# Performance work log

Hardware: AMD Instinct MI355X
Metric: run time of the kernel (lower is better)

## Reference

```python
import jax, jax.numpy as jnp
import numpy as np

C = 1024
H = 16
EPS = 1e-5

def layernorm(x, g, b):
    mu = jnp.mean(x, axis=-1, keepdims=True)
    var = jnp.var(x, axis=-1, keepdims=True)
    return (x - mu) * jax.lax.rsqrt(var + EPS) * g + b

def setup_inputs() -> dict:
    key = jax.random.key(0)
    ks = jax.random.split(key, 12)
    s = lambda fan: 1.0 / np.sqrt(fan)
    return {
        "x": jax.random.normal(ks[0], (2, 2048, C), jnp.float32),
        "W_qkv": jax.random.uniform(ks[1], (C, 3 * C), jnp.float32, -s(C), s(C)),
        "W_o": jax.random.uniform(ks[2], (C, C), jnp.float32, -s(C), s(C)),
        "b_o": jnp.zeros((C,), jnp.float32),
        "g1": jnp.ones((C,), jnp.float32),
        "beta1": jnp.zeros((C,), jnp.float32),
        "g2": jnp.ones((C,), jnp.float32),
        "beta2": jnp.zeros((C,), jnp.float32),
        "W_ff1": jax.random.uniform(ks[3], (C, 4 * C), jnp.float32, -s(C), s(C)),
        "b_ff1": jnp.zeros((4 * C,), jnp.float32),
        "W_ff2": jax.random.uniform(ks[4], (4 * C, C), jnp.float32, -s(4 * C), s(4 * C)),
        "b_ff2": jnp.zeros((C,), jnp.float32),
    }

def reference(x, W_qkv, W_o, b_o, g1, beta1, g2, beta2, W_ff1, b_ff1, W_ff2, b_ff2):
    B, T, _ = x.shape
    hd = C // H  # head dim
    # --- self-attention on norm1(x) ---
    h = layernorm(x, g1, beta1)
    qkv = h @ W_qkv                      # [B,T,3C]
    q, k, v = jnp.split(qkv, 3, axis=-1)
    reshp = lambda t: t.reshape(B, T, H, hd).transpose(0, 2, 1, 3)  # [B,H,T,hd]
    q, k, v = reshp(q), reshp(k), reshp(v)
    att = jnp.einsum("bhqd,bhkd->bhqk", q, k) * (hd ** -0.5)
    causal = jnp.tril(jnp.ones((T, T), bool))
    att = jnp.where(causal, att, -jnp.inf)
    att = jax.nn.softmax(att, axis=-1)
    out = jnp.einsum("bhqk,bhkd->bhqd", att, v)
    out = out.transpose(0, 2, 1, 3).reshape(B, T, C)
    x = x + out @ W_o + b_o
    # --- feed-forward on norm2(x) ---
    h = layernorm(x, g2, beta2)
    h = jax.nn.relu(h @ W_ff1 + b_ff1) @ W_ff2 + b_ff2
    return x + h
```

## Files before the change

### kernel.cpp

```cpp
#include <hip/hip_runtime.h>
#include <hip/hip_bf16.h>
#include <stdint.h>


typedef __attribute__((ext_vector_type(8))) short bf16x8;
typedef __attribute__((ext_vector_type(4))) float f32x4;

#define MFMA16(a, b, c) __builtin_amdgcn_mfma_f32_16x16x32_bf16((a), (b), (c), 0, 0, 0)

__device__ __forceinline__ void gload16(const void* g, void* l) {
    __builtin_amdgcn_global_load_lds(
        (const __attribute__((address_space(1))) char*)g,
        (__attribute__((address_space(3))) char*)l, 16, 0, 0);
}

__global__ __launch_bounds__(256) void tconv_k(const float* __restrict__ in,
                                               __hip_bfloat16* __restrict__ out,
                                               int K, int N) {
    __shared__ float tile[32][33];
    const int n0 = blockIdx.x * 32, k0 = blockIdx.y * 32;
    const int tx = threadIdx.x, ty = threadIdx.y;
    for (int i = ty; i < 32; i += 8)
        tile[i][tx] = in[(size_t)(k0 + i) * N + n0 + tx];
    __syncthreads();
    for (int i = ty; i < 32; i += 8)
        out[(size_t)(n0 + i) * K + k0 + tx] = __float2bfloat16(tile[tx][i]);
}

__global__ __launch_bounds__(256) void ln_k(const float* __restrict__ x,
                                            const float* __restrict__ g,
                                            const float* __restrict__ beta,
                                            __hip_bfloat16* __restrict__ out) {
    const int row = blockIdx.x;
    const int tid = threadIdx.x;
    float4 v = ((const float4*)(x + (size_t)row * 1024))[tid];
    float s  = v.x + v.y + v.z + v.w;
    float s2 = v.x * v.x + v.y * v.y + v.z * v.z + v.w * v.w;
    for (int off = 1; off < 64; off <<= 1) {
        s  += __shfl_xor(s,  off, 64);
        s2 += __shfl_xor(s2, off, 64);
    }
    __shared__ float ss[4], ss2[4];
    const int w = tid >> 6, lane = tid & 63;
    if (lane == 0) { ss[w] = s; ss2[w] = s2; }
    __syncthreads();
    s  = ss[0] + ss[1] + ss[2] + ss[3];
    s2 = ss2[0] + ss2[1] + ss2[2] + ss2[3];
    const float mu  = s * (1.0f / 1024.0f);
    const float var = s2 * (1.0f / 1024.0f) - mu * mu;
    const float rs  = rsqrtf(var + 1e-5f);
    float4 gv = ((const float4*)g)[tid];
    float4 bv = ((const float4*)beta)[tid];
    __hip_bfloat16* o = out + (size_t)row * 1024 + tid * 4;
    o[0] = __float2bfloat16((v.x - mu) * rs * gv.x + bv.x);
    o[1] = __float2bfloat16((v.y - mu) * rs * gv.y + bv.y);
    o[2] = __float2bfloat16((v.z - mu) * rs * gv.z + bv.z);
    o[3] = __float2bfloat16((v.w - mu) * rs * gv.w + bv.w);
}

template <int BIAS, int RELU, int RESID, int OUTBF>
__global__ __launch_bounds__(256, 2) void gemm_k(const __hip_bfloat16* __restrict__ A,
                                                 const __hip_bfloat16* __restrict__ Bt,
                                                 const float* __restrict__ bias,
                                                 const float* __restrict__ resid,
                                                 void* __restrict__ out,
                                                 int M, int N, int K) {
    __align__(16) __shared__ __hip_bfloat16 As[2][128 * 64];
    __align__(16) __shared__ __hip_bfloat16 Bs[2][128 * 64];

    const int tid  = threadIdx.x;
    const int lane = tid & 63, w = tid >> 6;
    const int wm = w >> 1, wn = w & 1;
    const int m0 = blockIdx.y * 128, n0 = blockIdx.x * 128;
    const int l16 = lane & 15, quad = lane >> 4;

    const int srw = lane >> 3;
    const int scn = ((lane & 7) - srw) & 7;

    const __hip_bfloat16* ga[4];
    const __hip_bfloat16* gb[4];
#pragma unroll
    for (int i = 0; i < 4; i++) {
        const int row = i * 32 + w * 8 + srw;
        ga[i] = A  + (size_t)(m0 + row) * K + scn * 8;
        gb[i] = Bt + (size_t)(n0 + row) * K + scn * 8;
    }

    int offA[2][4], offB[2][4];
#pragma unroll
    for (int s = 0; s < 2; s++)
#pragma unroll
        for (int t = 0; t < 4; t++) {
            const int rA = wm * 64 + t * 16 + l16;
            offA[s][t] = (rA * 8 + ((s * 4 + quad + (rA & 7)) & 7)) * 16;
            const int rB = wn * 64 + t * 16 + l16;
            offB[s][t] = (rB * 8 + ((s * 4 + quad + (rB & 7)) & 7)) * 16;
        }

    f32x4 acc[4][4] = {};

#pragma unroll
    for (int i = 0; i < 4; i++) {
        gload16(ga[i], As[0] + (i * 256 + w * 64) * 8);
        gload16(gb[i], Bs[0] + (i * 256 + w * 64) * 8);
        ga[i] += 64; gb[i] += 64;
    }

    const int niter = K >> 6;
    for (int it = 0; it < niter; it++) {
        const int buf = it & 1;
        __syncthreads();
        if (it + 1 < niter) {
#pragma unroll
            for (int i = 0; i < 4; i++) {
                gload16(ga[i], As[buf ^ 1] + (i * 256 + w * 64) * 8);
                gload16(gb[i], Bs[buf ^ 1] + (i * 256 + w * 64) * 8);
                ga[i] += 64; gb[i] += 64;
            }
        }

#pragma unroll
        for (int s = 0; s < 2; s++) {
            bf16x8 af[4], bfr[4];
#pragma unroll
            for (int t = 0; t < 4; t++) {
                af[t]  = *(const bf16x8*)((const char*)As[buf] + offA[s][t]);
                bfr[t] = *(const bf16x8*)((const char*)Bs[buf] + offB[s][t]);
            }
#pragma unroll
            for (int mt = 0; mt < 4; mt++)
#pragma unroll
                for (int nt = 0; nt < 4; nt++)
                    acc[mt][nt] = MFMA16(af[mt], bfr[nt], acc[mt][nt]);
        }
    }

#pragma unroll
    for (int mt = 0; mt < 4; mt++)
#pragma unroll
        for (int nt = 0; nt < 4; nt++) {
            const int row = m0 + wm * 64 + mt * 16 + quad * 4;
            const int col = n0 + wn * 64 + nt * 16 + l16;
            const float bv = BIAS ? bias[col] : 0.0f;
#pragma unroll
            for (int r = 0; r < 4; r++) {
                float v = acc[mt][nt][r] + bv;
                if (RELU) v = v > 0.0f ? v : 0.0f;
                const size_t idx = (size_t)(row + r) * N + col;
                if (RESID) v += resid[idx];
                if (OUTBF) ((__hip_bfloat16*)out)[idx] = __float2bfloat16(v);
                else       ((float*)out)[idx] = v;
            }
        }
}

template <int BIAS, int RELU, int RESID, int OUTBF>
__global__ __launch_bounds__(256, 3) void gemm64_k(const __hip_bfloat16* __restrict__ A,
                                                   const __hip_bfloat16* __restrict__ Bt,
                                                   const float* __restrict__ bias,
                                                   const float* __restrict__ resid,
                                                   void* __restrict__ out,
                                                   int M, int N, int K) {
    __align__(16) __shared__ __hip_bfloat16 As[2][128 * 64];
    __align__(16) __shared__ __hip_bfloat16 Bs[2][64 * 64];

    const int tid  = threadIdx.x;
    const int lane = tid & 63, w = tid >> 6;
    const int wm = w >> 1, wn = w & 1;
    const int m0 = blockIdx.y * 128, n0 = blockIdx.x * 64;
    const int l16 = lane & 15, quad = lane >> 4;

    const int srw = lane >> 3;
    const int scn = ((lane & 7) - srw) & 7;

    const __hip_bfloat16* ga[4];
    const __hip_bfloat16* gb[2];
#pragma unroll
    for (int i = 0; i < 4; i++)
        ga[i] = A + (size_t)(m0 + i * 32 + w * 8 + srw) * K + scn * 8;
#pragma unroll
    for (int i = 0; i < 2; i++)
        gb[i] = Bt + (size_t)(n0 + i * 32 + w * 8 + srw) * K + scn * 8;

    int offA[2][4], offB[2][2];
#pragma unroll
    for (int s = 0; s < 2; s++) {
#pragma unroll
        for (int t = 0; t < 4; t++) {
            const int rA = wm * 64 + t * 16 + l16;
            offA[s][t] = (rA * 8 + ((s * 4 + quad + (rA & 7)) & 7)) * 16;
        }
#pragma unroll
        for (int t = 0; t < 2; t++) {
            const int rB = wn * 32 + t * 16 + l16;
            offB[s][t] = (rB * 8 + ((s * 4 + quad + (rB & 7)) & 7)) * 16;
        }
    }

    f32x4 acc[4][2] = {};

#pragma unroll
    for (int i = 0; i < 4; i++) {
        gload16(ga[i], As[0] + (i * 256 + w * 64) * 8);
        ga[i] += 64;
    }
#pragma unroll
    for (int i = 0; i < 2; i++) {
        gload16(gb[i], Bs[0] + (i * 256 + w * 64) * 8);
        gb[i] += 64;
    }

    const int niter = K >> 6;
    for (int it = 0; it < niter; it++) {
        const int buf = it & 1;
        __syncthreads();
        if (it + 1 < niter) {
#pragma unroll
            for (int i = 0; i < 4; i++) {
                gload16(ga[i], As[buf ^ 1] + (i * 256 + w * 64) * 8);
                ga[i] += 64;
            }
#pragma unroll
            for (int i = 0; i < 2; i++) {
                gload16(gb[i], Bs[buf ^ 1] + (i * 256 + w * 64) * 8);
                gb[i] += 64;
            }
        }

#pragma unroll
        for (int s = 0; s < 2; s++) {
            bf16x8 af[4], bfr[2];
#pragma unroll
            for (int t = 0; t < 4; t++)
                af[t] = *(const bf16x8*)((const char*)As[buf] + offA[s][t]);
#pragma unroll
            for (int t = 0; t < 2; t++)
                bfr[t] = *(const bf16x8*)((const char*)Bs[buf] + offB[s][t]);
#pragma unroll
            for (int mt = 0; mt < 4; mt++)
#pragma unroll
                for (int nt = 0; nt < 2; nt++)
                    acc[mt][nt] = MFMA16(af[mt], bfr[nt], acc[mt][nt]);
        }
    }

#pragma unroll
    for (int mt = 0; mt < 4; mt++)
#pragma unroll
        for (int nt = 0; nt < 2; nt++) {
            const int row = m0 + wm * 64 + mt * 16 + quad * 4;
            const int col = n0 + wn * 32 + nt * 16 + l16;
            const float bv = BIAS ? bias[col] : 0.0f;
#pragma unroll
            for (int r = 0; r < 4; r++) {
                float v = acc[mt][nt][r] + bv;
                if (RELU) v = v > 0.0f ? v : 0.0f;
                const size_t idx = (size_t)(row + r) * N + col;
                if (RESID) v += resid[idx];
                if (OUTBF) ((__hip_bfloat16*)out)[idx] = __float2bfloat16(v);
                else       ((float*)out)[idx] = v;
            }
        }
}

__global__ __launch_bounds__(256) void vtrans_k(const __hip_bfloat16* __restrict__ qkv,
                                                __hip_bfloat16* __restrict__ vt) {
    const int T = 2048, C3 = 3072;
    const int bh = blockIdx.y, b = bh >> 4, h = bh & 15;
    const int t0 = blockIdx.x * 64;
    const int tx = threadIdx.x, ty = threadIdx.y;
    __shared__ __hip_bfloat16 tile[64][65];
#pragma unroll
    for (int j = 0; j < 16; j++) {
        const int tl = ty * 16 + j;
        tile[tl][tx] = qkv[(size_t)(b * T + t0 + tl) * C3 + 2048 + h * 64 + tx];
    }
    __syncthreads();
#pragma unroll
    for (int j = 0; j < 16; j++) {
        const int d = ty * 16 + j;
        vt[((size_t)bh * 64 + d) * 2048 + t0 + tx] = tile[tx][d];
    }
}

__global__ __launch_bounds__(256, 3) void attn_k(const __hip_bfloat16* __restrict__ qkv,
                                                 const __hip_bfloat16* __restrict__ vt,
                                                 __hip_bfloat16* __restrict__ outp) {
    const int T = 2048, C3 = 3072;
    const int bh = blockIdx.x, b = bh >> 4, h = bh & 15;
    const int qt = 31 - blockIdx.y;
    const int q0 = qt * 64;
    const int tid = threadIdx.x, lane = tid & 63, w = tid >> 6;
    const int l16 = lane & 15, quad = lane >> 4;

    __align__(16) __shared__ __hip_bfloat16 Ks[2][64 * 64];
    __align__(16) __shared__ __hip_bfloat16 Vs[2][64 * 64];
    __align__(16) __shared__ __hip_bfloat16 Pw[4][16 * 72];

    const float sc = 0.125f * 1.44269504f;
    bf16x8 qf0, qf1;
    {
        const __hip_bfloat16* qp =
            qkv + (size_t)(b * T + q0 + w * 16 + l16) * C3 + h * 64;
        bf16x8 a = *(const bf16x8*)(qp + quad * 8);
        bf16x8 c = *(const bf16x8*)(qp + 32 + quad * 8);
#pragma unroll
        for (int i = 0; i < 8; i++) {
            union { unsigned int u; float f; } ua, uc;
            ua.u = ((unsigned int)(unsigned short)a[i]) << 16;
            uc.u = ((unsigned int)(unsigned short)c[i]) << 16;
            qf0[i] = (short)(__bfloat16_as_ushort(__float2bfloat16(ua.f * sc)));
            qf1[i] = (short)(__bfloat16_as_ushort(__float2bfloat16(uc.f * sc)));
        }
    }

    const int srw = lane >> 3;
    const int scn = ((lane & 7) - srw) & 7;
    const __hip_bfloat16* kp[2];
    const __hip_bfloat16* vp[2];
#pragma unroll
    for (int i = 0; i < 2; i++) {
        const int row = i * 32 + w * 8 + srw;
        kp[i] = qkv + (size_t)(b * T + row) * C3 + 1024 + h * 64 + scn * 8;
        vp[i] = vt + ((size_t)bh * 64 + row) * 2048 + scn * 8;
    }

    int offK[2][4];
#pragma unroll
    for (int s = 0; s < 2; s++)
#pragma unroll
        for (int t = 0; t < 4; t++) {
            const int rr = t * 16 + l16;
            offK[s][t] = (rr * 8 + ((s * 4 + quad + (rr & 7)) & 7)) * 16;
        }

    f32x4 oacc[4] = {};
    float lpart[4] = {0.0f, 0.0f, 0.0f, 0.0f};

#pragma unroll
    for (int i = 0; i < 2; i++) {
        gload16(kp[i], Ks[0] + (i * 256 + w * 64) * 8);
        gload16(vp[i], Vs[0] + (i * 256 + w * 64) * 8);
    }

    for (int kt = 0; kt <= qt; kt++) {
        const int buf = kt & 1;
        __syncthreads();
        if (kt < qt) {
#pragma unroll
            for (int i = 0; i < 2; i++) {
                gload16(kp[i] + (size_t)(kt + 1) * 64 * C3,
                        Ks[buf ^ 1] + (i * 256 + w * 64) * 8);
                gload16(vp[i] + (kt + 1) * 64,
                        Vs[buf ^ 1] + (i * 256 + w * 64) * 8);
            }
        }

        f32x4 s4[4];
#pragma unroll
        for (int nt = 0; nt < 4; nt++) {
            bf16x8 kf0 = *(const bf16x8*)((const char*)Ks[buf] + offK[0][nt]);
            bf16x8 kf1 = *(const bf16x8*)((const char*)Ks[buf] + offK[1][nt]);
            f32x4 z = {};
            z = MFMA16(qf0, kf0, z);
            z = MFMA16(qf1, kf1, z);
            s4[nt] = z;
        }

        const bool diag = (kt == qt);
        const int myrow = w * 16 + quad * 4;
#pragma unroll
        for (int nt = 0; nt < 4; nt++) {
            const int col = nt * 16 + l16;
#pragma unroll
            for (int r = 0; r < 4; r++) {
                float p = exp2f(s4[nt][r]);
                if (diag && col > myrow + r) p = 0.0f;
                lpart[r] += p;
                Pw[w][(quad * 4 + r) * 72 + col] = __float2bfloat16(p);
            }
        }

        asm volatile("s_waitcnt lgkmcnt(0)" ::: "memory");

        bf16x8 pf0 = *(const bf16x8*)(&Pw[w][l16 * 72 + quad * 8]);
        bf16x8 pf1 = *(const bf16x8*)(&Pw[w][l16 * 72 + 32 + quad * 8]);
#pragma unroll
        for (int dt = 0; dt < 4; dt++) {
            bf16x8 vf0 = *(const bf16x8*)((const char*)Vs[buf] + offK[0][dt]);
            bf16x8 vf1 = *(const bf16x8*)((const char*)Vs[buf] + offK[1][dt]);
            oacc[dt] = MFMA16(pf0, vf0, oacc[dt]);
            oacc[dt] = MFMA16(pf1, vf1, oacc[dt]);
        }
    }

#pragma unroll
    for (int off = 1; off < 16; off <<= 1)
#pragma unroll
        for (int r = 0; r < 4; r++)
            lpart[r] += __shfl_xor(lpart[r], off, 64);

    float rl[4];
#pragma unroll
    for (int r = 0; r < 4; r++) rl[r] = 1.0f / lpart[r];
#pragma unroll
    for (int dt = 0; dt < 4; dt++)
#pragma unroll
        for (int r = 0; r < 4; r++) {
            const int row = q0 + w * 16 + quad * 4 + r;
            outp[(size_t)(b * T + row) * 1024 + h * 64 + dt * 16 + l16] =
                __float2bfloat16(oacc[dt][r] * rl[r]);
        }
}

extern "C" void kernel_launch(void* const* d_in, const int* in_sizes, int n_in,
                              void* d_out, int out_size, void* d_ws, size_t ws_size,
                              hipStream_t stream) {
    const float* x     = (const float*)d_in[0];
    const float* Wqkv  = (const float*)d_in[1];
    const float* Wo    = (const float*)d_in[2];
    const float* b_o   = (const float*)d_in[3];
    const float* g1    = (const float*)d_in[4];
    const float* beta1 = (const float*)d_in[5];
    const float* g2    = (const float*)d_in[6];
    const float* beta2 = (const float*)d_in[7];
    const float* Wff1  = (const float*)d_in[8];
    const float* bff1  = (const float*)d_in[9];
    const float* Wff2  = (const float*)d_in[10];
    const float* bff2  = (const float*)d_in[11];

    char* ws = (char*)d_ws;
    size_t off = 0;
    auto alloc = [&](size_t bytes) {
        void* p = ws + off;
        off += (bytes + 255) & ~(size_t)255;
        return p;
    };
    __hip_bfloat16* Wqkv_t = (__hip_bfloat16*)alloc(3072ULL * 1024 * 2);
    __hip_bfloat16* Wo_t   = (__hip_bfloat16*)alloc(1024ULL * 1024 * 2);
    __hip_bfloat16* Wff1_t = (__hip_bfloat16*)alloc(4096ULL * 1024 * 2);
    __hip_bfloat16* Wff2_t = (__hip_bfloat16*)alloc(1024ULL * 4096 * 2);
    __hip_bfloat16* h_bf   = (__hip_bfloat16*)alloc(4096ULL * 1024 * 2);
    __hip_bfloat16* qkv_bf = (__hip_bfloat16*)alloc(4096ULL * 3072 * 2);
    __hip_bfloat16* att_bf = (__hip_bfloat16*)alloc(4096ULL * 1024 * 2);
    float*          x2     = (float*)alloc(4096ULL * 1024 * 4);
    __hip_bfloat16* ff1_bf = qkv_bf;
    __hip_bfloat16* vt     = (__hip_bfloat16*)x2;

    const dim3 tb(32, 8);
    tconv_k<<<dim3(3072 / 32, 1024 / 32), tb, 0, stream>>>(Wqkv, Wqkv_t, 1024, 3072);
    tconv_k<<<dim3(1024 / 32, 1024 / 32), tb, 0, stream>>>(Wo,   Wo_t,   1024, 1024);
    tconv_k<<<dim3(4096 / 32, 1024 / 32), tb, 0, stream>>>(Wff1, Wff1_t, 1024, 4096);
    tconv_k<<<dim3(1024 / 32, 4096 / 32), tb, 0, stream>>>(Wff2, Wff2_t, 4096, 1024);

    ln_k<<<4096, 256, 0, stream>>>(x, g1, beta1, h_bf);
    gemm_k<0, 0, 0, 1><<<dim3(3072 / 128, 4096 / 128), 256, 0, stream>>>(
        h_bf, Wqkv_t, nullptr, nullptr, qkv_bf, 4096, 3072, 1024);
    vtrans_k<<<dim3(32, 32), dim3(64, 4), 0, stream>>>(qkv_bf, vt);
    attn_k<<<dim3(32, 32), 256, 0, stream>>>(qkv_bf, vt, att_bf);
    gemm64_k<1, 0, 1, 0><<<dim3(1024 / 64, 4096 / 128), 256, 0, stream>>>(
        att_bf, Wo_t, b_o, x, x2, 4096, 1024, 1024);
    ln_k<<<4096, 256, 0, stream>>>(x2, g2, beta2, h_bf);
    gemm_k<1, 1, 0, 1><<<dim3(4096 / 128, 4096 / 128), 256, 0, stream>>>(
        h_bf, Wff1_t, bff1, nullptr, ff1_bf, 4096, 4096, 1024);
    gemm64_k<1, 0, 1, 0><<<dim3(1024 / 64, 4096 / 128), 256, 0, stream>>>(
        ff1_bf, Wff2_t, bff2, x2, (float*)d_out, 4096, 1024, 4096);
}
```

Before: 340.6 us.

## Merge weight transpose kernels and add XCD-aware block swizzle to GEMMs

Folds the four weight transpose/convert launches into one kernel that dispatches on a flat block index, removing three kernel launches and their tail gaps. Both GEMM kernels now remap the flat block id so that consecutive tiles land on the same XCD, aiming for better L2 reuse of shared A/B panels across the chiplets. The remap only applies when the block count is a multiple of eight, and it adds some integer div/mod work per block.

```diff
diff --git a/kernel.cpp b/kernel.cpp
--- a/kernel.cpp
+++ b/kernel.cpp
@@ -14,11 +14,27 @@
         (__attribute__((address_space(3))) char*)l, 16, 0, 0);
 }
 
-__global__ __launch_bounds__(256) void tconv_k(const float* __restrict__ in,
-                                               __hip_bfloat16* __restrict__ out,
-                                               int K, int N) {
+__device__ __forceinline__ int xcd_swizzle(int flat, int nblk) {
+    if ((nblk & 7) == 0) {
+        const int per = nblk >> 3;
+        flat = (flat & 7) * per + (flat >> 3);
+    }
+    return flat;
+}
+
+__global__ __launch_bounds__(256) void tconv_all(
+    const float* __restrict__ w0, __hip_bfloat16* __restrict__ o0,
+    const float* __restrict__ w1, __hip_bfloat16* __restrict__ o1,
+    const float* __restrict__ w2, __hip_bfloat16* __restrict__ o2,
+    const float* __restrict__ w3, __hip_bfloat16* __restrict__ o3) {
     __shared__ float tile[32][33];
-    const int n0 = blockIdx.x * 32, k0 = blockIdx.y * 32;
+    const int f = blockIdx.x;
+    const float* in; __hip_bfloat16* out; int K, N, nx, t;
+    if (f < 3072)      { in = w0; out = o0; K = 1024; N = 3072; nx = 96;  t = f; }
+    else if (f < 4096) { in = w1; out = o1; K = 1024; N = 1024; nx = 32;  t = f - 3072; }
+    else if (f < 8192) { in = w2; out = o2; K = 1024; N = 4096; nx = 128; t = f - 4096; }
+    else               { in = w3; out = o3; K = 4096; N = 1024; nx = 32;  t = f - 8192; }
+    const int n0 = (t % nx) * 32, k0 = (t / nx) * 32;
     const int tx = threadIdx.x, ty = threadIdx.y;
     for (int i = ty; i < 32; i += 8)
         tile[i][tx] = in[(size_t)(k0 + i) * N + n0 + tx];
@@ -71,7 +87,9 @@
     const int tid  = threadIdx.x;
     const int lane = tid & 63, w = tid >> 6;
     const int wm = w >> 1, wn = w & 1;
-    const int m0 = blockIdx.y * 128, n0 = blockIdx.x * 128;
+    const int nbx = gridDim.x;
+    const int flat = xcd_swizzle(blockIdx.y * nbx + blockIdx.x, nbx * gridDim.y);
+    const int m0 = (flat / nbx) * 128, n0 = (flat % nbx) * 128;
     const int l16 = lane & 15, quad = lane >> 4;
 
     const int srw = lane >> 3;
@@ -167,7 +185,9 @@
     const int tid  = threadIdx.x;
     const int lane = tid & 63, w = tid >> 6;
     const int wm = w >> 1, wn = w & 1;
-    const int m0 = blockIdx.y * 128, n0 = blockIdx.x * 64;
+    const int nbx = gridDim.x;
+    const int flat = xcd_swizzle(blockIdx.y * nbx + blockIdx.x, nbx * gridDim.y);
+    const int m0 = (flat / nbx) * 128, n0 = (flat % nbx) * 64;
     const int l16 = lane & 15, quad = lane >> 4;
 
     const int srw = lane >> 3;
@@ -447,11 +467,8 @@
     __hip_bfloat16* ff1_bf = qkv_bf;
     __hip_bfloat16* vt     = (__hip_bfloat16*)x2;
 
-    const dim3 tb(32, 8);
-    tconv_k<<<dim3(3072 / 32, 1024 / 32), tb, 0, stream>>>(Wqkv, Wqkv_t, 1024, 3072);
-    tconv_k<<<dim3(1024 / 32, 1024 / 32), tb, 0, stream>>>(Wo,   Wo_t,   1024, 1024);
-    tconv_k<<<dim3(4096 / 32, 1024 / 32), tb, 0, stream>>>(Wff1, Wff1_t, 1024, 4096);
-    tconv_k<<<dim3(1024 / 32, 4096 / 32), tb, 0, stream>>>(Wff2, Wff2_t, 4096, 1024);
+    tconv_all<<<12288, dim3(32, 8), 0, stream>>>(Wqkv, Wqkv_t, Wo, Wo_t,
+                                                 Wff1, Wff1_t, Wff2, Wff2_t);
 
     ln_k<<<4096, 256, 0, stream>>>(x, g1, beta1, h_bf);
     gemm_k<0, 0, 0, 1><<<dim3(3072 / 128, 4096 / 128), 256, 0, stream>>>(
```

After: 331.4 us. -2.7%, faster.
